# Optimization experiments

Hardware: AMD Instinct MI355X
Metric: run time of the kernel (lower is better)

The kernel has to match this reference:

```python
import jax, jax.numpy as jnp
import numpy as np

IN_FEATURES = 4096
OUT_FEATURES = 11008
W_BITS = 4
GROUP_SIZE = 128
NUM_CHERRIES = 128                       # ceil(4096*0.03125)//8*8
NUM_NORMAL = IN_FEATURES - NUM_CHERRIES  # 3968
N_GROUPS = NUM_NORMAL // GROUP_SIZE      # 31
QROWS = NUM_NORMAL // 8 * W_BITS         # 1984 packed uint8 rows
QMIN = -(2 ** (W_BITS - 1))              # signed int4 min = -8
BATCH = 64


def setup_inputs() -> dict:
    key = jax.random.key(0)
    k1, k2, k3, k4, k5 = jax.random.split(key, 5)
    x = jax.random.normal(k1, (BATCH, IN_FEATURES), jnp.float32)
    # packed 4-bit weights: two nibbles per uint8, stored as [QROWS, out]
    qweight = jax.random.randint(k2, (QROWS, OUT_FEATURES), 0, 256, jnp.int32).astype(jnp.uint8)
    # per-group scales, stored transposed as [n_groups, out]
    scales = jax.random.uniform(k3, (N_GROUPS, OUT_FEATURES), jnp.float32, 0.005, 0.02)
    # full-precision outlier ('cherry') columns, stored as [num_cherries, out]
    cherry_weight = jax.random.normal(k4, (NUM_CHERRIES, OUT_FEATURES), jnp.float32) * 0.02
    rng = np.random.default_rng(0)
    cherry_indices = jnp.asarray(
        np.sort(rng.choice(IN_FEATURES, NUM_CHERRIES, replace=False)).astype(np.int32))
    bias = jax.random.normal(k5, (OUT_FEATURES,), jnp.float32) * 0.01
    return {"x": x, "qweight": qweight, "cherry_weight": cherry_weight,
            "cherry_indices": cherry_indices, "scales": scales, "bias": bias}


def _normal_indices(cherry_indices):
    # complement of cherry_indices, as in the torch scatter/nonzero construction
    mask = jnp.ones((IN_FEATURES,), dtype=bool).at[cherry_indices].set(False)
    return jnp.nonzero(mask, size=NUM_NORMAL)[0]  # static size -> jit ok


def reference(x, qweight, cherry_weight, cherry_indices, scales, bias):
    # --- unpack 4-bit weights (matches QuantLinear.unpack for w_bits=4) ---
    q = qweight.T                                    # [out, QROWS]
    nib = jnp.stack([q & 0xF, (q >> 4) & 0xF], axis=-1)  # low nibble first
    nib = nib.reshape(OUT_FEATURES, NUM_NORMAL)
    intw = nib.astype(jnp.int32) + QMIN              # signed int4 values
    # --- dequantize: repeat-interleave per-group scales along in dim ---
    s = jnp.repeat(scales.T, GROUP_SIZE, axis=1)     # [out, NUM_NORMAL]
    w_normal = intw.astype(s.dtype) * s              # dequantized normal weight
    # --- merge cherry outlier columns via column-gather on x (same math as
    #     scattering into a full [out, in] weight then x @ W.T) ---
    normal_idx = _normal_indices(cherry_indices)
    out = x[:, normal_idx] @ w_normal.T + x[:, cherry_indices] @ cherry_weight
    return out + bias
```

## Files before the change

kernel.cpp:

```cpp
#include <hip/hip_runtime.h>
#include <hip/hip_bf16.h>
#include <stdint.h>

#define IN_F 4096
#define OUT_F 11008
#define NUM_CH 128
#define NUM_NORM 3968
#define BATCH 64
#define KSPLIT 8
#define KCHUNK (IN_F / KSPLIT)
#define NSTEP (KCHUNK / 32)

typedef short short8 __attribute__((ext_vector_type(8)));
typedef float float4v __attribute__((ext_vector_type(4)));

__device__ __forceinline__ unsigned short f2bf(float f) {
    union { float f; unsigned u; } v; v.f = f;
    unsigned u = v.u;
    return (unsigned short)((u + 0x7FFFu + ((u >> 16) & 1u)) >> 16);
}

__device__ __forceinline__ unsigned pk_bf16(float lo, float hi) {
    __hip_bfloat162 h = __float22bfloat162_rn(make_float2(lo, hi));
    union { __hip_bfloat162 h; unsigned u; } c; c.h = h; return c.u;
}

__global__ __launch_bounds__(256) void init_out(
        const float* __restrict__ bias, float* __restrict__ out) {
    const int i = blockIdx.x * 256 + threadIdx.x;
    const int c = i % (OUT_F / 4);
    const float4v b4 = *reinterpret_cast<const float4v*>(bias + c * 4);
    reinterpret_cast<float4v*>(out)[i] = b4;
}

__global__ __launch_bounds__(256) void permute_x(
        const float* __restrict__ x, const int* __restrict__ cidx,
        unsigned short* __restrict__ xp) {
    int i = blockIdx.x * blockDim.x + threadIdx.x;
    int b = blockIdx.y;
    int lo = 0, hi = NUM_CH;
    while (lo < hi) { int mid = (lo + hi) >> 1; if (cidx[mid] < i) lo = mid + 1; else hi = mid; }
    bool isch = (lo < NUM_CH) && (cidx[lo] == i);
    int pos = isch ? (NUM_NORM + lo) : (i - lo);
    xp[b * IN_F + pos] = f2bf(x[b * IN_F + i]);
}

__global__ __launch_bounds__(256, 4) void qgemm(
        const unsigned short* __restrict__ xp, const int* __restrict__ qw,
        const float* __restrict__ cw, const float* __restrict__ scales,
        float* __restrict__ out) {
    const int tid  = threadIdx.x;
    const int wave = tid >> 6;
    const int lane = tid & 63;
    const int ln   = lane & 15;
    const int lq   = lane >> 4;

    const int nw    = blockIdx.x * 64 + wave * 16 + ln;
    const int kbase = blockIdx.y * KCHUNK;

    const int*   qcol = qw + nw;
    const float* scol = scales + nw;
    const float* ccol = cw + nw;

    float4v acc[4];
    #pragma unroll
    for (int s = 0; s < 4; ++s) acc[s] = (float4v){0.f, 0.f, 0.f, 0.f};

    int qn0, qn1, qn2, qn3; float scn;
    {
        const int rb = (kbase + lq * 8) >> 1;
        scn = scol[(size_t)(kbase >> 7) * OUT_F];
        qn0 = qcol[(size_t)(rb + 0) * OUT_F];
        qn1 = qcol[(size_t)(rb + 1) * OUT_F];
        qn2 = qcol[(size_t)(rb + 2) * OUT_F];
        qn3 = qcol[(size_t)(rb + 3) * OUT_F];
    }
    short8 a_cur[4];
    #pragma unroll
    for (int mt = 0; mt < 4; ++mt)
        a_cur[mt] = *reinterpret_cast<const short8*>(
            xp + (size_t)(mt * 16 + ln) * IN_F + kbase + lq * 8);

    for (int step = 0; step < NSTEP; ++step) {
        const int k0 = kbase + (step << 5);
        union { short8 s; unsigned u[4]; } bb;

        if (k0 < NUM_NORM) {
            const int q0 = qn0, q1 = qn1, q2 = qn2, q3 = qn3;
            const float sc = scn;
            const int kn = k0 + 32;
            if (step + 1 < NSTEP && kn < NUM_NORM) {
                const int rb = (kn + lq * 8) >> 1;
                scn = scol[(size_t)(kn >> 7) * OUT_F];
                qn0 = qcol[(size_t)(rb + 0) * OUT_F];
                qn1 = qcol[(size_t)(rb + 1) * OUT_F];
                qn2 = qcol[(size_t)(rb + 2) * OUT_F];
                qn3 = qcol[(size_t)(rb + 3) * OUT_F];
            }
            bb.u[0] = pk_bf16((float)((q0 & 0xF) - 8) * sc, (float)(((q0 >> 4) & 0xF) - 8) * sc);
            bb.u[1] = pk_bf16((float)((q1 & 0xF) - 8) * sc, (float)(((q1 >> 4) & 0xF) - 8) * sc);
            bb.u[2] = pk_bf16((float)((q2 & 0xF) - 8) * sc, (float)(((q2 >> 4) & 0xF) - 8) * sc);
            bb.u[3] = pk_bf16((float)((q3 & 0xF) - 8) * sc, (float)(((q3 >> 4) & 0xF) - 8) * sc);
        } else {
            const int kr = k0 + lq * 8 - NUM_NORM;
            float c[8];
            #pragma unroll
            for (int j = 0; j < 8; ++j) c[j] = ccol[(size_t)(kr + j) * OUT_F];
            #pragma unroll
            for (int r = 0; r < 4; ++r) bb.u[r] = pk_bf16(c[2 * r], c[2 * r + 1]);
        }

        const short8 a0 = a_cur[0], a1 = a_cur[1], a2 = a_cur[2], a3 = a_cur[3];
        if (step + 1 < NSTEP) {
            const int kn = k0 + 32;
            #pragma unroll
            for (int mt = 0; mt < 4; ++mt)
                a_cur[mt] = *reinterpret_cast<const short8*>(
                    xp + (size_t)(mt * 16 + ln) * IN_F + kn + lq * 8);
        }

        acc[0] = __builtin_amdgcn_mfma_f32_16x16x32_bf16(a0, bb.s, acc[0], 0, 0, 0);
        acc[1] = __builtin_amdgcn_mfma_f32_16x16x32_bf16(a1, bb.s, acc[1], 0, 0, 0);
        acc[2] = __builtin_amdgcn_mfma_f32_16x16x32_bf16(a2, bb.s, acc[2], 0, 0, 0);
        acc[3] = __builtin_amdgcn_mfma_f32_16x16x32_bf16(a3, bb.s, acc[3], 0, 0, 0);
    }

    #pragma unroll
    for (int mt = 0; mt < 4; ++mt) {
        #pragma unroll
        for (int r = 0; r < 4; ++r) {
            const int m = mt * 16 + (lq << 2) + r;
            atomicAdd(&out[(size_t)m * OUT_F + nw], acc[mt][r]);
        }
    }
}

extern "C" void kernel_launch(void* const* d_in, const int* in_sizes, int n_in,
                              void* d_out, int out_size, void* d_ws, size_t ws_size,
                              hipStream_t stream) {
    const float* x      = (const float*)d_in[0];
    const int*   qw     = (const int*)d_in[1];
    const float* cw     = (const float*)d_in[2];
    const int*   cidx   = (const int*)d_in[3];
    const float* scales = (const float*)d_in[4];
    const float* bias   = (const float*)d_in[5];
    float*       out    = (float*)d_out;
    unsigned short* xp  = (unsigned short*)d_ws;

    init_out<<<(BATCH * OUT_F / 4) / 256, 256, 0, stream>>>(bias, out);
    dim3 pgrid(IN_F / 256, BATCH);
    permute_x<<<pgrid, 256, 0, stream>>>(x, cidx, xp);
    qgemm<<<dim3(OUT_F / 64, KSPLIT), 256, 0, stream>>>(xp, qw, cw, scales, out);
}
```

Before: 193.1 us.

## Stage dequantized weights in double-buffered LDS with vectorized int4 loads

New measurement: 164.2 us. -15.0%, faster.

```diff
diff --git a/kernel.cpp b/kernel.cpp
--- a/kernel.cpp
+++ b/kernel.cpp
@@ -9,10 +9,12 @@
 #define BATCH 64
 #define KSPLIT 8
 #define KCHUNK (IN_F / KSPLIT)
-#define NSTEP (KCHUNK / 32)
+#define NMEGA (KCHUNK / 128)
+#define BS 136
 
 typedef short short8 __attribute__((ext_vector_type(8)));
 typedef float float4v __attribute__((ext_vector_type(4)));
+typedef int int4v __attribute__((ext_vector_type(4)));
 
 __device__ __forceinline__ unsigned short f2bf(float f) {
     union { float f; unsigned u; } v; v.f = f;
@@ -49,88 +51,109 @@
         const unsigned short* __restrict__ xp, const int* __restrict__ qw,
         const float* __restrict__ cw, const float* __restrict__ scales,
         float* __restrict__ out) {
+    __shared__ unsigned short Bt[2][64][BS];
+
     const int tid  = threadIdx.x;
     const int wave = tid >> 6;
     const int lane = tid & 63;
     const int ln   = lane & 15;
     const int lq   = lane >> 4;
+    const int n0    = blockIdx.x * 64;
+    const int kbase = blockIdx.y * KCHUNK;
+    const int tcol = (tid & 15) << 2;
+    const int trow = tid >> 4;
 
-    const int nw    = blockIdx.x * 64 + wave * 16 + ln;
-    const int kbase = blockIdx.y * KCHUNK;
-
-    const int*   qcol = qw + nw;
-    const float* scol = scales + nw;
-    const float* ccol = cw + nw;
+    const int*   qbase = qw + n0 + tcol;
+    const float* sbase = scales + n0 + tcol;
+    const float* cbase = cw + n0 + tcol;
 
     float4v acc[4];
     #pragma unroll
     for (int s = 0; s < 4; ++s) acc[s] = (float4v){0.f, 0.f, 0.f, 0.f};
 
-    int qn0, qn1, qn2, qn3; float scn;
+    int4v qcur[4]; float4v scur;
     {
-        const int rb = (kbase + lq * 8) >> 1;
-        scn = scol[(size_t)(kbase >> 7) * OUT_F];
-        qn0 = qcol[(size_t)(rb + 0) * OUT_F];
-        qn1 = qcol[(size_t)(rb + 1) * OUT_F];
-        qn2 = qcol[(size_t)(rb + 2) * OUT_F];
-        qn3 = qcol[(size_t)(rb + 3) * OUT_F];
+        const int rb = (kbase >> 1) + 4 * trow;
+        #pragma unroll
+        for (int i = 0; i < 4; ++i)
+            qcur[i] = *reinterpret_cast<const int4v*>(qbase + (size_t)(rb + i) * OUT_F);
+        scur = *reinterpret_cast<const float4v*>(sbase + (size_t)(kbase >> 7) * OUT_F);
     }
-    short8 a_cur[4];
-    #pragma unroll
-    for (int mt = 0; mt < 4; ++mt)
-        a_cur[mt] = *reinterpret_cast<const short8*>(
-            xp + (size_t)(mt * 16 + ln) * IN_F + kbase + lq * 8);
 
-    for (int step = 0; step < NSTEP; ++step) {
-        const int k0 = kbase + (step << 5);
-        union { short8 s; unsigned u[4]; } bb;
+    for (int s = 0; s < NMEGA; ++s) {
+        const int k0 = kbase + s * 128;
+        unsigned short (*buf)[BS] = Bt[s & 1];
 
         if (k0 < NUM_NORM) {
-            const int q0 = qn0, q1 = qn1, q2 = qn2, q3 = qn3;
-            const float sc = scn;
-            const int kn = k0 + 32;
-            if (step + 1 < NSTEP && kn < NUM_NORM) {
-                const int rb = (kn + lq * 8) >> 1;
-                scn = scol[(size_t)(kn >> 7) * OUT_F];
-                qn0 = qcol[(size_t)(rb + 0) * OUT_F];
-                qn1 = qcol[(size_t)(rb + 1) * OUT_F];
-                qn2 = qcol[(size_t)(rb + 2) * OUT_F];
-                qn3 = qcol[(size_t)(rb + 3) * OUT_F];
+            const int4v q0 = qcur[0], q1 = qcur[1], q2 = qcur[2], q3 = qcur[3];
+            const float4v sc = scur;
+            const int kn = k0 + 128;
+            if (s + 1 < NMEGA && kn < NUM_NORM) {
+                const int rb = (kn >> 1) + 4 * trow;
+                #pragma unroll
+                for (int i = 0; i < 4; ++i)
+                    qcur[i] = *reinterpret_cast<const int4v*>(qbase + (size_t)(rb + i) * OUT_F);
+                scur = *reinterpret_cast<const float4v*>(sbase + (size_t)(kn >> 7) * OUT_F);
             }
-            bb.u[0] = pk_bf16((float)((q0 & 0xF) - 8) * sc, (float)(((q0 >> 4) & 0xF) - 8) * sc);
-            bb.u[1] = pk_bf16((float)((q1 & 0xF) - 8) * sc, (float)(((q1 >> 4) & 0xF) - 8) * sc);
-            bb.u[2] = pk_bf16((float)((q2 & 0xF) - 8) * sc, (float)(((q2 >> 4) & 0xF) - 8) * sc);
-            bb.u[3] = pk_bf16((float)((q3 & 0xF) - 8) * sc, (float)(((q3 >> 4) & 0xF) - 8) * sc);
+            const int4v qq[4] = {q0, q1, q2, q3};
+            #pragma unroll
+            for (int cc = 0; cc < 4; ++cc) {
+                union { short8 v; unsigned u[4]; } wv;
+                const float s1 = sc[cc];
+                #pragma unroll
+                for (int i = 0; i < 4; ++i) {
+                    const int q = qq[i][cc];
+                    wv.u[i] = pk_bf16((float)((q & 0xF) - 8) * s1,
+                                      (float)(((q >> 4) & 0xF) - 8) * s1);
+                }
+                *reinterpret_cast<short8*>(&buf[tcol + cc][trow * 8]) = wv.v;
+            }
         } else {
-            const int kr = k0 + lq * 8 - NUM_NORM;
-            float c[8];
+            float4v ch[8];
             #pragma unroll
-            for (int j = 0; j < 8; ++j) c[j] = ccol[(size_t)(kr + j) * OUT_F];
+            for (int j = 0; j < 8; ++j)
+                ch[j] = *reinterpret_cast<const float4v*>(
+                    cbase + (size_t)(8 * trow + j) * OUT_F);
             #pragma unroll
-            for (int r = 0; r < 4; ++r) bb.u[r] = pk_bf16(c[2 * r], c[2 * r + 1]);
+            for (int cc = 0; cc < 4; ++cc) {
+                union { short8 v; unsigned u[4]; } wv;
+                #pragma unroll
+                for (int m = 0; m < 4; ++m)
+                    wv.u[m] = pk_bf16(ch[2 * m][cc], ch[2 * m + 1][cc]);
+                *reinterpret_cast<short8*>(&buf[tcol + cc][trow * 8]) = wv.v;
+            }
         }
 
-        const short8 a0 = a_cur[0], a1 = a_cur[1], a2 = a_cur[2], a3 = a_cur[3];
-        if (step + 1 < NSTEP) {
-            const int kn = k0 + 32;
-            #pragma unroll
-            for (int mt = 0; mt < 4; ++mt)
-                a_cur[mt] = *reinterpret_cast<const short8*>(
-                    xp + (size_t)(mt * 16 + ln) * IN_F + kn + lq * 8);
+        __syncthreads();
+
+        const unsigned short* xprow =
+            xp + (size_t)((wave << 4) + ln) * IN_F + k0 + (lq << 3);
+        const short8 a0 = *reinterpret_cast<const short8*>(xprow);
+        const short8 a1 = *reinterpret_cast<const short8*>(xprow + 32);
+        const short8 a2 = *reinterpret_cast<const short8*>(xprow + 64);
+        const short8 a3 = *reinterpret_cast<const short8*>(xprow + 96);
+
+        #pragma unroll
+        for (int st = 0; st < 4; ++st) {
+            const unsigned short* bp = &buf[(st << 4) + ln][lq << 3];
+            acc[st] = __builtin_amdgcn_mfma_f32_16x16x32_bf16(
+                a0, *reinterpret_cast<const short8*>(bp), acc[st], 0, 0, 0);
+            acc[st] = __builtin_amdgcn_mfma_f32_16x16x32_bf16(
+                a1, *reinterpret_cast<const short8*>(bp + 32), acc[st], 0, 0, 0);
+            acc[st] = __builtin_amdgcn_mfma_f32_16x16x32_bf16(
+                a2, *reinterpret_cast<const short8*>(bp + 64), acc[st], 0, 0, 0);
+            acc[st] = __builtin_amdgcn_mfma_f32_16x16x32_bf16(
+                a3, *reinterpret_cast<const short8*>(bp + 96), acc[st], 0, 0, 0);
         }
-
-        acc[0] = __builtin_amdgcn_mfma_f32_16x16x32_bf16(a0, bb.s, acc[0], 0, 0, 0);
-        acc[1] = __builtin_amdgcn_mfma_f32_16x16x32_bf16(a1, bb.s, acc[1], 0, 0, 0);
-        acc[2] = __builtin_amdgcn_mfma_f32_16x16x32_bf16(a2, bb.s, acc[2], 0, 0, 0);
-        acc[3] = __builtin_amdgcn_mfma_f32_16x16x32_bf16(a3, bb.s, acc[3], 0, 0, 0);
     }
 
     #pragma unroll
-    for (int mt = 0; mt < 4; ++mt) {
+    for (int st = 0; st < 4; ++st) {
+        const int n = n0 + (st << 4) + ln;
         #pragma unroll
         for (int r = 0; r < 4; ++r) {
-            const int m = mt * 16 + (lq << 2) + r;
-            atomicAdd(&out[(size_t)m * OUT_F + nw], acc[mt][r]);
+            const int m = (wave << 4) + (lq << 2) + r;
+            atomicAdd(&out[(size_t)m * OUT_F + n], acc[st][r]);
         }
     }
 }
```
